# Optimization experiments

Hardware: AMD Instinct MI355X
Metric: run time of the kernel (lower is better)

## Reference

```python
import jax, jax.numpy as jnp
import numpy as np

EMBED_DIM, NUM_HEADS, LOCAL_SIZE = 256, 4, 15
HEAD_DIM = EMBED_DIM // NUM_HEADS
SCALING = float(HEAD_DIM) ** -0.5


def get_overlap_segments(x, window_size):
    # x: (n, t, d) -> (n, t, window_size, d), zero-padded local windows centered at each position
    n, t, d = x.shape
    p = (window_size - 1) // 2
    xp = jnp.pad(x, ((0, 0), (p, p), (0, 0)))
    idx = jnp.arange(t)[:, None] + jnp.arange(window_size)[None, :]  # (t, w)
    return xp[:, idx]


def setup_inputs():
    key = jax.random.key(0)
    ks = jax.random.split(key, 4)
    B, W, F = 4, 64, 4096
    T = W + F
    x = jax.random.normal(ks[0], (B, T, EMBED_DIM), dtype=jnp.float32)
    # block one-hot frame->window assignment (each window owns F//W consecutive frames)
    assign = jnp.repeat(jnp.arange(W), F // W)
    wm = jnp.broadcast_to(jax.nn.one_hot(assign, W, dtype=jnp.float32).T[None], (B, W, F))
    W_qkv = jax.random.normal(ks[1], (EMBED_DIM, 3 * EMBED_DIM), jnp.float32) * 0.02
    b_qkv = jnp.zeros((3 * EMBED_DIM,), jnp.float32)
    W_out = jax.random.normal(ks[2], (EMBED_DIM, EMBED_DIM), jnp.float32) * 0.02
    b_out = jnp.zeros((EMBED_DIM,), jnp.float32)
    return {"x": x, "window_mapping": wm, "W_qkv": W_qkv, "b_qkv": b_qkv,
            "W_out": W_out, "b_out": b_out}


def _to_heads(z, b, t):
    # (b, t, E) -> (b*H, t, d), matching torch transpose/reshape ordering (b outer, h inner)
    return z.reshape(b, t, NUM_HEADS, HEAD_DIM).transpose(0, 2, 1, 3).reshape(b * NUM_HEADS, t, HEAD_DIM)


def reference(x, window_mapping, W_qkv, b_qkv, W_out, b_out):
    b, t, e = x.shape
    Wn, Fn = window_mapping.shape[1], window_mapping.shape[2]
    qkv = x @ W_qkv + b_qkv
    Q, K, V = jnp.split(qkv, 3, axis=-1)
    Q = Q * SCALING
    wtok = _to_heads(x[:, :Wn], b, Wn)            # (n, W, d) raw word tokens
    Qh = _to_heads(Q, b, t)[:, Wn:]               # (n, F, d)
    Kh = _to_heads(K, b, t)[:, Wn:]
    Vh = _to_heads(V, b, t)[:, Wn:]
    wm = jnp.broadcast_to(window_mapping[:, None], (b, NUM_HEADS, Wn, Fn)).reshape(b * NUM_HEADS, Wn, Fn)
    # scatter each window's word token to its frames
    expa = jnp.einsum('nwd,nwf->nfd', wtok, wm)   # (n, F, d)
    Kseg = get_overlap_segments(Kh, LOCAL_SIZE)   # (n, F, w, d)
    Vseg = get_overlap_segments(Vh, LOCAL_SIZE)
    Kcat = jnp.concatenate([expa[:, :, None], Kseg], axis=2)  # (n, F, 1+w, d)
    scores = jnp.einsum('nfd,nfwd->nfw', Qh, Kcat)            # (n, F, 1+w)
    # word-token weight: softmax across frames within each window chunk (F % W == 0, no pad)
    chunk = Fn // Wn
    w_wtok = jax.nn.softmax(scores[:, :, 0].reshape(-1, Wn, chunk), axis=-1).reshape(-1, Fn)
    # local-window weights: softmax over the window axis
    w_fea = jax.nn.softmax(scores[:, :, 1:], axis=-1)
    attn = jnp.concatenate([w_wtok[:, :, None], w_fea], axis=2)  # (n, F, 1+w)
    Vcat = jnp.concatenate([expa[:, :, None], Vseg], axis=2)
    out_fea = jnp.einsum('nfw,nfwd->nfd', attn, Vcat)            # (n, F, d)
    out = jnp.concatenate([wtok, out_fea], axis=1)               # (n, T, d)
    out = out.reshape(b, NUM_HEADS, t, HEAD_DIM).transpose(0, 2, 1, 3).reshape(b, t, e)
    return out @ W_out + b_out
```

## Files before the change

kernel.cpp:

```cpp
#include <hip/hip_runtime.h>


#define QN 4194304ull

typedef _Float16 h8 __attribute__((ext_vector_type(8)));
typedef _Float16 h4 __attribute__((ext_vector_type(4)));
typedef _Float16 h2 __attribute__((ext_vector_type(2)));
typedef float f32x16 __attribute__((ext_vector_type(16)));

__global__ __launch_bounds__(256) void conv_small(
    const float* __restrict__ x,
    const float* __restrict__ Wq, const float* __restrict__ Wo,
    _Float16* __restrict__ wqth, _Float16* __restrict__ woth,
    _Float16* __restrict__ xh) {
  const int g = blockIdx.x, tid = threadIdx.x;
  if (g < 768) {
    int o = g * 256 + tid;
    int n = o >> 8, k = o & 255;
    wqth[o] = (_Float16)Wq[(size_t)k * 768 + n];
  } else if (g < 1024) {
    int o = (g - 768) * 256 + tid;
    int n = o >> 8, k = o & 255;
    woth[o] = (_Float16)Wo[(size_t)k * 256 + n];
  } else {
    size_t base = (size_t)(g - 1024) * 4096 + (size_t)tid * 4;
#pragma unroll
    for (int c = 0; c < 4; ++c) {
      float4 v = *(const float4*)(x + base + c * 1024);
      h4 hv = {(_Float16)v.x, (_Float16)v.y, (_Float16)v.z, (_Float16)v.w};
      *(h4*)(xh + base + c * 1024) = hv;
    }
  }
}

__global__ __launch_bounds__(256) void qkv_mfma(
    const _Float16* __restrict__ xh, const _Float16* __restrict__ wth,
    const float* __restrict__ bq,
    _Float16* __restrict__ Qh, _Float16* __restrict__ Kh,
    _Float16* __restrict__ Vh) {
  __shared__ _Float16 Ah[128][40], Bh[128][40];
  const int tid = threadIdx.x;
  const int wave = tid >> 6, lane = tid & 63;
  const int ln = lane & 31, half = lane >> 5;
  const int mw = (wave & 1) * 64, nw = (wave >> 1) * 64;
  const int m0 = blockIdx.x * 128, n0 = blockIdx.y * 128;

  const int sr = tid >> 1, scq = (tid & 1) * 16;
  const int am = m0 + sr;
  const size_t arow =
      ((size_t)((am >> 12) * 4160 + 64 + (am & 4095))) * 256 + scq;
  const size_t brow = (size_t)(n0 + sr) * 256 + scq;

  float4 rah0, rah1, rbh0, rbh1;
  auto QLOAD = [&](int k0_) {
    rah0 = *(const float4*)(xh + arow + k0_);
    rah1 = *(const float4*)(xh + arow + k0_ + 8);
    rbh0 = *(const float4*)(wth + brow + k0_);
    rbh1 = *(const float4*)(wth + brow + k0_ + 8);
  };

  QLOAD(0);
  f32x16 acc[2][2] = {};

  for (int it = 0; it < 8; ++it) {
    __syncthreads();
    *(float4*)&Ah[sr][scq] = rah0;
    *(float4*)&Ah[sr][scq + 8] = rah1;
    *(float4*)&Bh[sr][scq] = rbh0;
    *(float4*)&Bh[sr][scq + 8] = rbh1;
    __syncthreads();
    if (it < 7) QLOAD((it + 1) * 32);
#pragma unroll
    for (int ks = 0; ks < 2; ++ks) {
      const int kc = ks * 16 + half * 8;
      h8 a0 = *(const h8*)&Ah[mw + ln][kc];
      h8 a1 = *(const h8*)&Ah[mw + 32 + ln][kc];
      h8 b0 = *(const h8*)&Bh[nw + ln][kc];
      h8 b1 = *(const h8*)&Bh[nw + 32 + ln][kc];
      acc[0][0] = __builtin_amdgcn_mfma_f32_32x32x16_f16(a0, b0, acc[0][0], 0, 0, 0);
      acc[0][1] = __builtin_amdgcn_mfma_f32_32x32x16_f16(a0, b1, acc[0][1], 0, 0, 0);
      acc[1][0] = __builtin_amdgcn_mfma_f32_32x32x16_f16(a1, b0, acc[1][0], 0, 0, 0);
      acc[1][1] = __builtin_amdgcn_mfma_f32_32x32x16_f16(a1, b1, acc[1][1], 0, 0, 0);
    }
  }

#pragma unroll
  for (int ni = 0; ni < 2; ++ni) {
    const int c = n0 + nw + ni * 32 + ln;
    const int which = c >> 8, e = c & 255;
    const int h = e >> 6, d = e & 63;
    _Float16* dst = (which == 0) ? Qh : (which == 1) ? Kh : Vh;
    const float sc2 = (which == 0) ? 0.125f : 1.0f;
    const float bias = bq[c];
#pragma unroll
    for (int mi = 0; mi < 2; ++mi) {
      const int rb = m0 + mw + mi * 32 + 4 * half;
#pragma unroll
      for (int reg = 0; reg < 16; ++reg) {
        int rr = rb + (reg & 3) + 8 * (reg >> 2);
        int b2 = rr >> 12, f2 = rr & 4095;
        dst[(((size_t)(b2 * 4 + h)) * 4096 + f2) * 64 + d] =
            (_Float16)((acc[mi][ni][reg] + bias) * sc2);
      }
    }
  }
}

__global__ __launch_bounds__(256) void attn_fused(
    const _Float16* __restrict__ Qh, const _Float16* __restrict__ Kh,
    const _Float16* __restrict__ Vh, const _Float16* __restrict__ xh,
    _Float16* __restrict__ OFh) {
  __shared__ _Float16 Ks[78][72];
  __shared__ _Float16 Vs[78][72];
  __shared__ float s0s[64];
  __shared__ float red[2];
  const int tid = threadIdx.x;
  const int w = blockIdx.x;
  const int n = blockIdx.y;
  const int f0 = w * 64;
  const int b = n >> 2, h = n & 3;

  for (int idx = tid; idx < 78 * 8; idx += 256) {
    int rr = idx >> 3, c = (idx & 7) * 8;
    int g = f0 - 7 + rr;
    h8 k8 = {}, v8 = {};
    if (g >= 0 && g < 4096) {
      size_t base = ((size_t)n * 4096 + g) * 64 + c;
      k8 = *(const h8*)(Kh + base);
      v8 = *(const h8*)(Vh + base);
    }
    *(h8*)&Ks[rr][c] = k8;
    *(h8*)&Vs[rr][c] = v8;
  }
  __syncthreads();

  const int i = tid >> 2, q = tid & 3;
  const size_t qbase = ((size_t)n * 4096 + f0 + i) * 64 + q * 16;
  h8 qh0 = *(const h8*)(Qh + qbase);
  h8 qh1 = *(const h8*)(Qh + qbase + 8);
  const size_t wbase = ((size_t)(b * 4160 + w)) * 256 + h * 64 + q * 16;
  h8 e0 = *(const h8*)(xh + wbase);
  h8 e1 = *(const h8*)(xh + wbase + 8);

  auto dot8 = [](h8 a, h8 bb, float s) {
    s = __builtin_amdgcn_fdot2((h2){a.s0, a.s1}, (h2){bb.s0, bb.s1}, s, false);
    s = __builtin_amdgcn_fdot2((h2){a.s2, a.s3}, (h2){bb.s2, bb.s3}, s, false);
    s = __builtin_amdgcn_fdot2((h2){a.s4, a.s5}, (h2){bb.s4, bb.s5}, s, false);
    s = __builtin_amdgcn_fdot2((h2){a.s6, a.s7}, (h2){bb.s6, bb.s7}, s, false);
    return s;
  };

  float s0 = dot8(qh1, e1, dot8(qh0, e0, 0.f));
  s0 += __shfl_xor(s0, 1);
  s0 += __shfl_xor(s0, 2);

  float sj[15];
#pragma unroll
  for (int j = 0; j < 15; ++j) {
    h8 k0 = *(const h8*)&Ks[i + j][q * 16];
    h8 k1 = *(const h8*)&Ks[i + j][q * 16 + 8];
    float s = dot8(qh1, k1, dot8(qh0, k0, 0.f));
    s += __shfl_xor(s, 1);
    s += __shfl_xor(s, 2);
    sj[j] = s;
  }

  if (q == 0) s0s[i] = s0;
  __syncthreads();
  if (tid < 64) {
    float v = s0s[tid];
    float m = v;
    for (int o = 1; o < 64; o <<= 1) m = fmaxf(m, __shfl_xor(m, o));
    float ee = __expf(v - m);
    float s = ee;
    for (int o = 1; o < 64; o <<= 1) s += __shfl_xor(s, o);
    if (tid == 0) { red[0] = m; red[1] = s; }
  }
  __syncthreads();
  const float wt = __expf(s0 - red[0]) / red[1];

  float mx = sj[0];
#pragma unroll
  for (int j = 1; j < 15; ++j) mx = fmaxf(mx, sj[j]);
  float pj[15], den = 0.f;
#pragma unroll
  for (int j = 0; j < 15; ++j) { pj[j] = __expf(sj[j] - mx); den += pj[j]; }
  const float inv = 1.0f / den;

  float o[16];
#pragma unroll
  for (int k = 0; k < 8; ++k) o[k] = wt * (float)e0[k];
#pragma unroll
  for (int k = 0; k < 8; ++k) o[8 + k] = wt * (float)e1[k];
#pragma unroll
  for (int j = 0; j < 15; ++j) {
    float wj = pj[j] * inv;
    h8 v0 = *(const h8*)&Vs[i + j][q * 16];
    h8 v1 = *(const h8*)&Vs[i + j][q * 16 + 8];
    o[0] = fmaf(wj, (float)v0.s0, o[0]);
    o[1] = fmaf(wj, (float)v0.s1, o[1]);
    o[2] = fmaf(wj, (float)v0.s2, o[2]);
    o[3] = fmaf(wj, (float)v0.s3, o[3]);
    o[4] = fmaf(wj, (float)v0.s4, o[4]);
    o[5] = fmaf(wj, (float)v0.s5, o[5]);
    o[6] = fmaf(wj, (float)v0.s6, o[6]);
    o[7] = fmaf(wj, (float)v0.s7, o[7]);
    o[8] = fmaf(wj, (float)v1.s0, o[8]);
    o[9] = fmaf(wj, (float)v1.s1, o[9]);
    o[10] = fmaf(wj, (float)v1.s2, o[10]);
    o[11] = fmaf(wj, (float)v1.s3, o[11]);
    o[12] = fmaf(wj, (float)v1.s4, o[12]);
    o[13] = fmaf(wj, (float)v1.s5, o[13]);
    o[14] = fmaf(wj, (float)v1.s6, o[14]);
    o[15] = fmaf(wj, (float)v1.s7, o[15]);
  }
  _Float16 oh[16];
#pragma unroll
  for (int dd = 0; dd < 16; ++dd) oh[dd] = (_Float16)o[dd];
  *(float4*)(OFh + qbase) = *(float4*)&oh[0];
  *(float4*)(OFh + qbase + 8) = *(float4*)&oh[8];
}

__global__ __launch_bounds__(256) void out_mfma(
    const _Float16* __restrict__ xh, const _Float16* __restrict__ ofh,
    const _Float16* __restrict__ wth, const float* __restrict__ bo,
    float* __restrict__ out) {
  __shared__ _Float16 Ah[64][72], Bh[64][72];
  const int tid = threadIdx.x;
  const int wave = tid >> 6, lane = tid & 63;
  const int ln = lane & 31, half = lane >> 5;
  const int mw = (wave & 1) * 32, nw = (wave >> 1) * 32;
  const int m0 = blockIdx.x * 64, n0 = blockIdx.y * 64;
  const int sr = tid >> 2, sc4 = (tid & 3) * 16;
  const int m = m0 + sr;
  const int b = m / 4160, tt = m % 4160;
  const bool useX = (tt < 64);
  const size_t xrow = ((size_t)(b * 4160 + tt)) * 256 + sc4;
  const long obase = ((long)(b * 4) * 4096 + (tt - 64)) * 64 + sc4;
  const size_t bbase = (size_t)(n0 + sr) * 256 + sc4;

  float4 ra0, ra1, rb0, rb1;
  auto OLOAD = [&](int k0_) {
    if (useX) {
      ra0 = *(const float4*)(xh + xrow + k0_);
      ra1 = *(const float4*)(xh + xrow + k0_ + 8);
    } else {
      size_t o_ = (size_t)(obase + (long)(k0_ >> 6) * 262144);
      ra0 = *(const float4*)(ofh + o_);
      ra1 = *(const float4*)(ofh + o_ + 8);
    }
    rb0 = *(const float4*)(wth + bbase + k0_);
    rb1 = *(const float4*)(wth + bbase + k0_ + 8);
  };

  OLOAD(0);
  f32x16 acc = {};
  for (int it = 0; it < 4; ++it) {
    __syncthreads();
    *(float4*)&Ah[sr][sc4] = ra0;
    *(float4*)&Ah[sr][sc4 + 8] = ra1;
    *(float4*)&Bh[sr][sc4] = rb0;
    *(float4*)&Bh[sr][sc4 + 8] = rb1;
    __syncthreads();
    if (it < 3) OLOAD((it + 1) * 64);
#pragma unroll
    for (int ks = 0; ks < 4; ++ks) {
      const int kc = ks * 16 + half * 8;
      h8 ah = *(const h8*)&Ah[mw + ln][kc];
      h8 bh = *(const h8*)&Bh[nw + ln][kc];
      acc = __builtin_amdgcn_mfma_f32_32x32x16_f16(ah, bh, acc, 0, 0, 0);
    }
  }
  const int c = n0 + nw + ln;
  const float bias = bo[c];
  const int rb = m0 + mw + 4 * half;
#pragma unroll
  for (int reg = 0; reg < 16; ++reg) {
    int rr = rb + (reg & 3) + 8 * (reg >> 2);
    out[(size_t)rr * 256 + c] = acc[reg] + bias;
  }
}

extern "C" void kernel_launch(void* const* d_in, const int* in_sizes, int n_in,
                              void* d_out, int out_size, void* d_ws, size_t ws_size,
                              hipStream_t stream) {
  const float* x  = (const float*)d_in[0];
  const float* Wq = (const float*)d_in[2];
  const float* bq = (const float*)d_in[3];
  const float* Wo = (const float*)d_in[4];
  const float* bo = (const float*)d_in[5];
  float* out = (float*)d_out;

  _Float16* Qh   = (_Float16*)d_ws;
  _Float16* Kh   = Qh + QN;
  _Float16* Vh   = Kh + QN;
  _Float16* OFh  = Vh + QN;
  _Float16* Wqth = OFh + QN;
  _Float16* Woth = Wqth + 196608;
  _Float16* xh   = Woth + 65536;

  conv_small<<<dim3(2064), 256, 0, stream>>>(x, Wq, Wo, Wqth, Woth, xh);
  qkv_mfma<<<dim3(128, 6), 256, 0, stream>>>(xh, Wqth, bq, Qh, Kh, Vh);
  attn_fused<<<dim3(64, 16), 256, 0, stream>>>(Qh, Kh, Vh, xh, OFh);
  out_mfma<<<dim3(260, 4), 256, 0, stream>>>(xh, OFh, Woth, bo, out);
}
```

Measured before the change: 115.9 us.

## Drop LDS staging in QKV and output GEMMs, load MFMA operands directly

Both GEMM kernels now skip shared-memory tiling and barriers. Each lane loads its MFMA fragments (8 halves) straight from global memory, counting on L1/L2 for reuse across waves. The output projection also moves from 64x64 to 128x128 tiles with four accumulators per wave, which halves the grid in each dimension. This removes LDS round trips and syncs, but each global load now fetches only 16 bytes per lane with strided rows, so less of each access is coalesced and there is no explicit prefetch.

```diff
diff --git a/kernel.cpp b/kernel.cpp
--- a/kernel.cpp
+++ b/kernel.cpp
@@ -38,50 +38,32 @@
     const float* __restrict__ bq,
     _Float16* __restrict__ Qh, _Float16* __restrict__ Kh,
     _Float16* __restrict__ Vh) {
-  __shared__ _Float16 Ah[128][40], Bh[128][40];
   const int tid = threadIdx.x;
   const int wave = tid >> 6, lane = tid & 63;
   const int ln = lane & 31, half = lane >> 5;
   const int mw = (wave & 1) * 64, nw = (wave >> 1) * 64;
   const int m0 = blockIdx.x * 128, n0 = blockIdx.y * 128;
 
-  const int sr = tid >> 1, scq = (tid & 1) * 16;
-  const int am = m0 + sr;
-  const size_t arow =
-      ((size_t)((am >> 12) * 4160 + 64 + (am & 4095))) * 256 + scq;
-  const size_t brow = (size_t)(n0 + sr) * 256 + scq;
-
-  float4 rah0, rah1, rbh0, rbh1;
-  auto QLOAD = [&](int k0_) {
-    rah0 = *(const float4*)(xh + arow + k0_);
-    rah1 = *(const float4*)(xh + arow + k0_ + 8);
-    rbh0 = *(const float4*)(wth + brow + k0_);
-    rbh1 = *(const float4*)(wth + brow + k0_ + 8);
-  };
-
-  QLOAD(0);
+  const int am0 = m0 + mw + ln, am1 = am0 + 32;
+  const size_t ar0 =
+      ((size_t)((am0 >> 12) * 4160 + 64 + (am0 & 4095))) * 256 + half * 8;
+  const size_t ar1 =
+      ((size_t)((am1 >> 12) * 4160 + 64 + (am1 & 4095))) * 256 + half * 8;
+  const size_t br0 = (size_t)(n0 + nw + ln) * 256 + half * 8;
+  const size_t br1 = (size_t)(n0 + nw + 32 + ln) * 256 + half * 8;
+
   f32x16 acc[2][2] = {};
-
-  for (int it = 0; it < 8; ++it) {
-    __syncthreads();
-    *(float4*)&Ah[sr][scq] = rah0;
-    *(float4*)&Ah[sr][scq + 8] = rah1;
-    *(float4*)&Bh[sr][scq] = rbh0;
-    *(float4*)&Bh[sr][scq + 8] = rbh1;
-    __syncthreads();
-    if (it < 7) QLOAD((it + 1) * 32);
-#pragma unroll
-    for (int ks = 0; ks < 2; ++ks) {
-      const int kc = ks * 16 + half * 8;
-      h8 a0 = *(const h8*)&Ah[mw + ln][kc];
-      h8 a1 = *(const h8*)&Ah[mw + 32 + ln][kc];
-      h8 b0 = *(const h8*)&Bh[nw + ln][kc];
-      h8 b1 = *(const h8*)&Bh[nw + 32 + ln][kc];
-      acc[0][0] = __builtin_amdgcn_mfma_f32_32x32x16_f16(a0, b0, acc[0][0], 0, 0, 0);
-      acc[0][1] = __builtin_amdgcn_mfma_f32_32x32x16_f16(a0, b1, acc[0][1], 0, 0, 0);
-      acc[1][0] = __builtin_amdgcn_mfma_f32_32x32x16_f16(a1, b0, acc[1][0], 0, 0, 0);
-      acc[1][1] = __builtin_amdgcn_mfma_f32_32x32x16_f16(a1, b1, acc[1][1], 0, 0, 0);
-    }
+#pragma unroll 4
+  for (int kk = 0; kk < 16; ++kk) {
+    const int ko = kk * 16;
+    h8 a0 = *(const h8*)(xh + ar0 + ko);
+    h8 a1 = *(const h8*)(xh + ar1 + ko);
+    h8 b0 = *(const h8*)(wth + br0 + ko);
+    h8 b1 = *(const h8*)(wth + br1 + ko);
+    acc[0][0] = __builtin_amdgcn_mfma_f32_32x32x16_f16(a0, b0, acc[0][0], 0, 0, 0);
+    acc[0][1] = __builtin_amdgcn_mfma_f32_32x32x16_f16(a0, b1, acc[0][1], 0, 0, 0);
+    acc[1][0] = __builtin_amdgcn_mfma_f32_32x32x16_f16(a1, b0, acc[1][0], 0, 0, 0);
+    acc[1][1] = __builtin_amdgcn_mfma_f32_32x32x16_f16(a1, b1, acc[1][1], 0, 0, 0);
   }
 
 #pragma unroll
@@ -225,59 +207,56 @@
     const _Float16* __restrict__ xh, const _Float16* __restrict__ ofh,
     const _Float16* __restrict__ wth, const float* __restrict__ bo,
     float* __restrict__ out) {
-  __shared__ _Float16 Ah[64][72], Bh[64][72];
   const int tid = threadIdx.x;
   const int wave = tid >> 6, lane = tid & 63;
   const int ln = lane & 31, half = lane >> 5;
-  const int mw = (wave & 1) * 32, nw = (wave >> 1) * 32;
-  const int m0 = blockIdx.x * 64, n0 = blockIdx.y * 64;
-  const int sr = tid >> 2, sc4 = (tid & 3) * 16;
-  const int m = m0 + sr;
-  const int b = m / 4160, tt = m % 4160;
-  const bool useX = (tt < 64);
-  const size_t xrow = ((size_t)(b * 4160 + tt)) * 256 + sc4;
-  const long obase = ((long)(b * 4) * 4096 + (tt - 64)) * 64 + sc4;
-  const size_t bbase = (size_t)(n0 + sr) * 256 + sc4;
-
-  float4 ra0, ra1, rb0, rb1;
-  auto OLOAD = [&](int k0_) {
-    if (useX) {
-      ra0 = *(const float4*)(xh + xrow + k0_);
-      ra1 = *(const float4*)(xh + xrow + k0_ + 8);
-    } else {
-      size_t o_ = (size_t)(obase + (long)(k0_ >> 6) * 262144);
-      ra0 = *(const float4*)(ofh + o_);
-      ra1 = *(const float4*)(ofh + o_ + 8);
-    }
-    rb0 = *(const float4*)(wth + bbase + k0_);
-    rb1 = *(const float4*)(wth + bbase + k0_ + 8);
-  };
-
-  OLOAD(0);
-  f32x16 acc = {};
-  for (int it = 0; it < 4; ++it) {
-    __syncthreads();
-    *(float4*)&Ah[sr][sc4] = ra0;
-    *(float4*)&Ah[sr][sc4 + 8] = ra1;
-    *(float4*)&Bh[sr][sc4] = rb0;
-    *(float4*)&Bh[sr][sc4 + 8] = rb1;
-    __syncthreads();
-    if (it < 3) OLOAD((it + 1) * 64);
-#pragma unroll
-    for (int ks = 0; ks < 4; ++ks) {
-      const int kc = ks * 16 + half * 8;
-      h8 ah = *(const h8*)&Ah[mw + ln][kc];
-      h8 bh = *(const h8*)&Bh[nw + ln][kc];
-      acc = __builtin_amdgcn_mfma_f32_32x32x16_f16(ah, bh, acc, 0, 0, 0);
-    }
-  }
-  const int c = n0 + nw + ln;
-  const float bias = bo[c];
-  const int rb = m0 + mw + 4 * half;
-#pragma unroll
-  for (int reg = 0; reg < 16; ++reg) {
-    int rr = rb + (reg & 3) + 8 * (reg >> 2);
-    out[(size_t)rr * 256 + c] = acc[reg] + bias;
+  const int mw = (wave & 1) * 64, nw = (wave >> 1) * 64;
+  const int m0 = blockIdx.x * 128, n0 = blockIdx.y * 128;
+
+  const int m_[2] = {m0 + mw + ln, m0 + mw + 32 + ln};
+  size_t xb_[2];
+  long ob_[2];
+  bool useX_[2];
+#pragma unroll
+  for (int r = 0; r < 2; ++r) {
+    const int b = m_[r] / 4160, tt = m_[r] % 4160;
+    useX_[r] = (tt < 64);
+    xb_[r] = ((size_t)(b * 4160 + tt)) * 256 + half * 8;
+    ob_[r] = ((long)(b * 4) * 4096 + (tt - 64)) * 64 + half * 8;
+  }
+  const size_t br0 = (size_t)(n0 + nw + ln) * 256 + half * 8;
+  const size_t br1 = (size_t)(n0 + nw + 32 + ln) * 256 + half * 8;
+
+  f32x16 acc[2][2] = {};
+#pragma unroll 4
+  for (int kk = 0; kk < 16; ++kk) {
+    const int ko = kk * 16;
+    const long oo = (long)(kk >> 2) * 262144 + (kk & 3) * 16;
+    const _Float16* ap0 = useX_[0] ? (xh + xb_[0] + ko) : (ofh + ob_[0] + oo);
+    const _Float16* ap1 = useX_[1] ? (xh + xb_[1] + ko) : (ofh + ob_[1] + oo);
+    h8 a0 = *(const h8*)ap0;
+    h8 a1 = *(const h8*)ap1;
+    h8 b0 = *(const h8*)(wth + br0 + ko);
+    h8 b1 = *(const h8*)(wth + br1 + ko);
+    acc[0][0] = __builtin_amdgcn_mfma_f32_32x32x16_f16(a0, b0, acc[0][0], 0, 0, 0);
+    acc[0][1] = __builtin_amdgcn_mfma_f32_32x32x16_f16(a0, b1, acc[0][1], 0, 0, 0);
+    acc[1][0] = __builtin_amdgcn_mfma_f32_32x32x16_f16(a1, b0, acc[1][0], 0, 0, 0);
+    acc[1][1] = __builtin_amdgcn_mfma_f32_32x32x16_f16(a1, b1, acc[1][1], 0, 0, 0);
+  }
+
+#pragma unroll
+  for (int ni = 0; ni < 2; ++ni) {
+    const int c = n0 + nw + ni * 32 + ln;
+    const float bias = bo[c];
+#pragma unroll
+    for (int mi = 0; mi < 2; ++mi) {
+      const int rb = m0 + mw + mi * 32 + 4 * half;
+#pragma unroll
+      for (int reg = 0; reg < 16; ++reg) {
+        int rr = rb + (reg & 3) + 8 * (reg >> 2);
+        out[(size_t)rr * 256 + c] = acc[mi][ni][reg] + bias;
+      }
+    }
   }
 }
 
@@ -302,5 +281,5 @@
   conv_small<<<dim3(2064), 256, 0, stream>>>(x, Wq, Wo, Wqth, Woth, xh);
   qkv_mfma<<<dim3(128, 6), 256, 0, stream>>>(xh, Wqth, bq, Qh, Kh, Vh);
   attn_fused<<<dim3(64, 16), 256, 0, stream>>>(Qh, Kh, Vh, xh, OFh);
-  out_mfma<<<dim3(260, 4), 256, 0, stream>>>(xh, OFh, Woth, bo, out);
-}
+  out_mfma<<<dim3(130, 2), 256, 0, stream>>>(xh, OFh, Woth, bo, out);
+}
```

New measurement: 137.5 us. 1.19x slower.
